# Optimization experiments

Measured on AMD Instinct MI355X. Metric: run time of the kernel, lower is better.

Reference implementation:

```python
import jax, jax.numpy as jnp
import numpy as np


def setup_inputs() -> dict:
    key = jax.random.key(0)
    ks = jax.random.split(key, 6)
    B, C, W, H = 8, 512, 64, 64
    return {
        "x": jax.random.normal(ks[0], (B, C, W, H), dtype=jnp.float32),
        "proj_query": jax.random.normal(ks[1], (C, W, H), dtype=jnp.float32),
        "key_w": jax.random.normal(ks[2], (C, C), dtype=jnp.float32) * 0.02,
        "key_b": jax.random.normal(ks[3], (C,), dtype=jnp.float32) * 0.02,
        "value_w": jax.random.normal(ks[4], (C, C), dtype=jnp.float32) * 0.02,
        "value_b": jax.random.normal(ks[5], (C,), dtype=jnp.float32) * 0.02,
        "gamma": jnp.ones((1,), dtype=jnp.float32),
    }


def reference(x, proj_query, key_w, key_b, value_w, value_b, gamma):
    B, C, W, H = x.shape
    N = W * H
    # fixed memory query: (C, N); torch builds B x N x C via permute
    q = proj_query.reshape(C, N)
    # 1x1 convs == per-pixel channel matmuls
    k = jnp.einsum('oc,bchw->bohw', key_w, x) + key_b[None, :, None, None]
    v = jnp.einsum('oc,bchw->bohw', value_w, x) + value_b[None, :, None, None]
    k = k.reshape(B, C, N)
    v = v.reshape(B, C, N)
    # energy = bmm(key [B,C,N], query^T [N,C]) -> B x C x C (channel attention)
    energy = jnp.einsum('bcn,dn->bcd', k, q)
    attention = jax.nn.softmax(energy, axis=-1)
    # out = bmm(attention^T [B,C,C], value [B,C,N]) -> B x C x N
    out = jnp.einsum('bdc,bdn->bcn', attention, v)
    out = out.reshape(B, C, W, H)
    return gamma * out + x
```

## Files before the change

kernel.cpp:

```cpp
#include <hip/hip_runtime.h>

typedef unsigned short u16;
typedef unsigned int u32;
typedef _Float16 f16x8 __attribute__((ext_vector_type(8)));
typedef float f32x4 __attribute__((ext_vector_type(4)));

#define LDST 40

__device__ __forceinline__ u16 f2h(float f) {
  union { _Float16 h; u16 u; } c; c.h = (_Float16)f; return c.u;
}
__device__ __forceinline__ float h2f(u16 v) {
  union { u16 u; _Float16 h; } c; c.u = v; return (float)c.h;
}

__device__ __forceinline__ f32x4 mfma16(f16x8 a, f16x8 b, f32x4 c) {
  return __builtin_amdgcn_mfma_f32_16x16x32_f16(a, b, c, 0, 0, 0);
}

__device__ __forceinline__ void ld8f(const float* s, u16* o) {
  float4 a = *(const float4*)s;
  float4 b = *(const float4*)(s + 4);
  o[0] = f2h(a.x); o[1] = f2h(a.y); o[2] = f2h(a.z); o[3] = f2h(a.w);
  o[4] = f2h(b.x); o[5] = f2h(b.y); o[6] = f2h(b.z); o[7] = f2h(b.w);
}

template<int TM, int TN, bool NNB>
__device__ __forceinline__ void gemm_core(const u16* A, int lda, const u16* B, int ldb,
                                          int ksteps, u16* sA, u16* sB, f32x4 acc[TM][TN]) {
  const int t = threadIdx.x;
  const int lane = t & 63, wave = t >> 6;
  const int wm = wave >> 1, wn = wave & 1;
  const int m16 = lane & 15, q4 = lane >> 4;
  constexpr int BM = TM * 32, BN = TN * 32;

  for (int kt = 0; kt < ksteps; ++kt) {
    __syncthreads();
#pragma unroll
    for (int p = 0; p < BM / 64; ++p) {
      int flat = (p * 256 + t) * 8;
      int row = flat >> 5, col = flat & 31;
      *(int4*)&sA[row * LDST + col] = *(const int4*)&A[(size_t)row * lda + col];
    }
    if constexpr (!NNB) {
#pragma unroll
      for (int p = 0; p < BN / 64; ++p) {
        int flat = (p * 256 + t) * 8;
        int row = flat >> 5, col = flat & 31;
        *(int4*)&sB[row * LDST + col] = *(const int4*)&B[(size_t)row * ldb + col];
      }
    } else {
      int kk = (t >> 4) * 2, nn = (t & 15) * 8;
      const u16* src = B + (size_t)kk * ldb + nn;
      u16 a0[8], a1[8];
      *(int4*)a0 = *(const int4*)src;
      *(int4*)a1 = *(const int4*)(src + ldb);
#pragma unroll
      for (int e = 0; e < 8; ++e) {
        int n = nn + e;
        int kf = kk ^ (((n >> 3) & 3) << 3);
        *(u32*)&sB[n * LDST + kf] = (u32)a0[e] | ((u32)a1[e] << 16);
      }
    }
    __syncthreads();

    f16x8 af[TM], bv[TN];
#pragma unroll
    for (int i = 0; i < TM; ++i)
      af[i] = *(const f16x8*)&sA[(wm * TM * 16 + i * 16 + m16) * LDST + q4 * 8];
#pragma unroll
    for (int j = 0; j < TN; ++j) {
      int n = wn * TN * 16 + j * 16 + m16;
      int kf = NNB ? ((q4 * 8) ^ (((n >> 3) & 3) << 3)) : (q4 * 8);
      bv[j] = *(const f16x8*)&sB[n * LDST + kf];
    }
#pragma unroll
    for (int i = 0; i < TM; ++i)
#pragma unroll
      for (int j = 0; j < TN; ++j)
        acc[i][j] = mfma16(af[i], bv[j], acc[i][j]);

    A += 32;
    B += NNB ? (size_t)32 * ldb : (size_t)32;
  }
}

__global__ __launch_bounds__(256) void cvt_x_kernel(const float* __restrict__ x, u16* __restrict__ xh) {
  size_t i = ((size_t)blockIdx.x * 256 + threadIdx.x) * 8;
  u16 o[8];
  ld8f(x + i, o);
  *(int4*)&xh[i] = *(int4*)o;
}

__global__ __launch_bounds__(256) void cvt_q_kernel(const float* __restrict__ q, u16* __restrict__ qh,
                                                    float* __restrict__ qs) {
  int row = blockIdx.x, t = threadIdx.x;
  float s = 0.f;
#pragma unroll
  for (int p = 0; p < 2; ++p) {
    size_t i = (size_t)row * 4096 + p * 2048 + t * 8;
    u16 o[8];
    ld8f(q + i, o);
#pragma unroll
    for (int e = 0; e < 8; ++e) s += h2f(o[e]);
    *(int4*)&qh[i] = *(int4*)o;
  }
  for (int off = 32; off; off >>= 1) s += __shfl_xor(s, off);
  __shared__ float wsum[4];
  if ((t & 63) == 0) wsum[t >> 6] = s;
  __syncthreads();
  if (t == 0) qs[row] = wsum[0] + wsum[1] + wsum[2] + wsum[3];
}

__global__ __launch_bounds__(256) void prep_kernel(const float* __restrict__ vw, u16* __restrict__ vwT,
                                                   const float* __restrict__ kw, u16* __restrict__ kwh,
                                                   float* __restrict__ beta) {
  int blk = blockIdx.x, t = threadIdx.x;
  if (blk < 256) {
    __shared__ u16 sT[32 * 33];
    int bx = blk & 15, by = blk >> 4;
#pragma unroll
    for (int p = 0; p < 4; ++p) {
      int idx = p * 256 + t; int r = idx >> 5, c = idx & 31;
      sT[r * 33 + c] = f2h(vw[(size_t)(by * 32 + r) * 512 + bx * 32 + c]);
    }
    __syncthreads();
#pragma unroll
    for (int p = 0; p < 4; ++p) {
      int idx = p * 256 + t; int r = idx >> 5, c = idx & 31;
      vwT[(size_t)(bx * 32 + r) * 512 + by * 32 + c] = sT[c * 33 + r];
    }
  } else if (blk < 384) {
    size_t i = ((size_t)(blk - 256) * 256 + t) * 8;
    u16 o[8];
    ld8f(kw + i, o);
    *(int4*)&kwh[i] = *(int4*)o;
  } else {
    for (int i = t; i < 4096; i += 256) beta[i] = 0.f;
  }
}

__global__ __launch_bounds__(256) void sgemm_kernel(const u16* __restrict__ qh, const u16* __restrict__ xh,
                                                    u16* __restrict__ Sh) {
  __shared__ u16 sA[64 * LDST], sB[64 * LDST];
  int rt = blockIdx.x, jt = blockIdx.y;
  f32x4 acc[2][2];
#pragma unroll
  for (int i = 0; i < 2; ++i)
#pragma unroll
    for (int j = 0; j < 2; ++j) acc[i][j] = (f32x4){0.f, 0.f, 0.f, 0.f};
  gemm_core<2, 2, false>(qh + (size_t)jt * 64 * 4096, 4096,
                         xh + (size_t)rt * 64 * 4096, 4096, 128, sA, sB, acc);

  const int t = threadIdx.x, lane = t & 63, wave = t >> 6;
  const int wm = wave >> 1, wn = wave & 1, m16 = lane & 15, q4 = lane >> 4;
  int b = (rt * 64) >> 9, o0 = (rt * 64) & 511;
  u16* Ob = Sh + (size_t)b * 262144;
#pragma unroll
  for (int i = 0; i < 2; ++i)
#pragma unroll
    for (int j = 0; j < 2; ++j)
#pragma unroll
      for (int r = 0; r < 4; ++r) {
        int y = jt * 64 + wm * 32 + i * 16 + q4 * 4 + r;
        int o = o0 + wn * 32 + j * 16 + m16;
        Ob[(size_t)y * 512 + o] = f2h(acc[i][j][r]);
      }
}

__global__ __launch_bounds__(256) void egemm_kernel(const u16* __restrict__ kwh, const u16* __restrict__ Sh,
                                                    float* __restrict__ E) {
  __shared__ u16 sA[64 * LDST], sB[64 * LDST];
  int xt = blockIdx.x >> 3, yt = blockIdx.x & 7, b = blockIdx.y;
  f32x4 acc[2][2];
#pragma unroll
  for (int i = 0; i < 2; ++i)
#pragma unroll
    for (int j = 0; j < 2; ++j) acc[i][j] = (f32x4){0.f, 0.f, 0.f, 0.f};
  gemm_core<2, 2, false>(kwh + (size_t)xt * 64 * 512, 512,
                         Sh + (size_t)b * 262144 + (size_t)yt * 64 * 512, 512, 16, sA, sB, acc);

  const int t = threadIdx.x, lane = t & 63, wave = t >> 6;
  const int wm = wave >> 1, wn = wave & 1, m16 = lane & 15, q4 = lane >> 4;
  float* O = E + ((size_t)b * 512 + xt * 64) * 512 + yt * 64;
#pragma unroll
  for (int i = 0; i < 2; ++i)
#pragma unroll
    for (int j = 0; j < 2; ++j)
#pragma unroll
      for (int r = 0; r < 4; ++r) {
        int row = wm * 32 + i * 16 + q4 * 4 + r;
        int col = wn * 32 + j * 16 + m16;
        O[(size_t)row * 512 + col] = acc[i][j][r];
      }
}

__global__ __launch_bounds__(256) void softmax_kernel(const float* __restrict__ E, const float* __restrict__ qs,
                                                      const float* __restrict__ kb, const float* __restrict__ vb,
                                                      u16* __restrict__ attT, float* __restrict__ beta) {
  __shared__ float sE[16 * 516];
  __shared__ float sM[16], sS[16];
  int i0 = blockIdx.x * 16, b = blockIdx.y, t = threadIdx.x;
  const float* Eb = E + ((size_t)b * 512 + i0) * 512;
  for (int ch = 0; ch < 32; ++ch) {
    int idx = ch * 256 + t;
    int row = idx >> 9, col = idx & 511;
    sE[row * 516 + col] = Eb[(size_t)row * 512 + col] + kb[i0 + row] * qs[col];
  }
  __syncthreads();
  {
    int row = t >> 4, sub = t & 15;
    float mx = -1e30f;
    for (int ii = 0; ii < 32; ++ii) mx = fmaxf(mx, sE[row * 516 + sub + ii * 16]);
    for (int off = 8; off; off >>= 1) mx = fmaxf(mx, __shfl_xor(mx, off));
    float sm = 0.f;
    for (int ii = 0; ii < 32; ++ii) sm += __expf(sE[row * 516 + sub + ii * 16] - mx);
    for (int off = 8; off; off >>= 1) sm += __shfl_xor(sm, off);
    if (sub == 0) { sM[row] = mx; sS[row] = 1.f / sm; }
  }
  __syncthreads();
  float vbr = vb[i0 + (t & 15)];
  u16* Ob = attT + (size_t)b * 262144;
  for (int ch = 0; ch < 32; ++ch) {
    int idx = ch * 256 + t;
    int r = idx & 15, j = idx >> 4;
    float a = __expf(sE[r * 516 + j] - sM[r]) * sS[r];
    Ob[(size_t)j * 512 + i0 + r] = f2h(a);
    float part = a * vbr;
    for (int off = 8; off; off >>= 1) part += __shfl_xor(part, off);
    if (r == 0) atomicAdd(&beta[b * 512 + j], part);
  }
}

__global__ __launch_bounds__(256) void wgemm_kernel(const u16* __restrict__ attT, const u16* __restrict__ vwT,
                                                    u16* __restrict__ W) {
  __shared__ u16 sA[64 * LDST], sB[64 * LDST];
  int ct = blockIdx.x >> 3, ot = blockIdx.x & 7, b = blockIdx.y;
  f32x4 acc[2][2];
#pragma unroll
  for (int i = 0; i < 2; ++i)
#pragma unroll
    for (int j = 0; j < 2; ++j) acc[i][j] = (f32x4){0.f, 0.f, 0.f, 0.f};
  gemm_core<2, 2, false>(attT + (size_t)b * 262144 + (size_t)ct * 64 * 512, 512,
                         vwT + (size_t)ot * 64 * 512, 512, 16, sA, sB, acc);

  const int t = threadIdx.x, lane = t & 63, wave = t >> 6;
  const int wm = wave >> 1, wn = wave & 1, m16 = lane & 15, q4 = lane >> 4;
  u16* O = W + (size_t)b * 262144 + (size_t)(ct * 64) * 512 + ot * 64;
#pragma unroll
  for (int i = 0; i < 2; ++i)
#pragma unroll
    for (int j = 0; j < 2; ++j)
#pragma unroll
      for (int r = 0; r < 4; ++r) {
        int row = wm * 32 + i * 16 + q4 * 4 + r;
        int col = wn * 32 + j * 16 + m16;
        O[(size_t)row * 512 + col] = f2h(acc[i][j][r]);
      }
}

__global__ __launch_bounds__(256) void outgemm_kernel(const u16* __restrict__ W, const u16* __restrict__ xh,
                                                      const float* __restrict__ x, const float* __restrict__ beta,
                                                      const float* __restrict__ gm, float* __restrict__ out) {
  __shared__ u16 sA[128 * LDST], sB[128 * LDST];
  int nt = blockIdx.x, ct = blockIdx.y, b = blockIdx.z;
  f32x4 acc[4][4];
#pragma unroll
  for (int i = 0; i < 4; ++i)
#pragma unroll
    for (int j = 0; j < 4; ++j) acc[i][j] = (f32x4){0.f, 0.f, 0.f, 0.f};
  gemm_core<4, 4, true>(W + (size_t)b * 262144 + (size_t)ct * 128 * 512, 512,
                        xh + (size_t)b * 2097152 + nt * 128, 4096, 16, sA, sB, acc);

  const int t = threadIdx.x, lane = t & 63, wave = t >> 6;
  const int wm = wave >> 1, wn = wave & 1, m16 = lane & 15, q4 = lane >> 4;
  float g = gm[0];
#pragma unroll
  for (int i = 0; i < 4; ++i)
#pragma unroll
    for (int j = 0; j < 4; ++j)
#pragma unroll
      for (int r = 0; r < 4; ++r) {
        int c = ct * 128 + wm * 64 + i * 16 + q4 * 4 + r;
        int n = nt * 128 + wn * 64 + j * 16 + m16;
        size_t idx = (size_t)b * 2097152 + (size_t)c * 4096 + n;
        out[idx] = g * (acc[i][j][r] + beta[b * 512 + c]) + x[idx];
      }
}

extern "C" void kernel_launch(void* const* d_in, const int* in_sizes, int n_in,
                              void* d_out, int out_size, void* d_ws, size_t ws_size,
                              hipStream_t stream) {
  const float* x  = (const float*)d_in[0];
  const float* pq = (const float*)d_in[1];
  const float* kw = (const float*)d_in[2];
  const float* kb = (const float*)d_in[3];
  const float* vw = (const float*)d_in[4];
  const float* vb = (const float*)d_in[5];
  const float* gm = (const float*)d_in[6];
  float* out = (float*)d_out;

  char* ws = (char*)d_ws;
  u16*   xh   = (u16*)(ws);
  u16*   qh   = (u16*)(ws + (32ull << 20));
  u16*   Sh   = (u16*)(ws + (36ull << 20));
  u16*   W    = (u16*)(ws + (36ull << 20));
  float* E    = (float*)(ws + (40ull << 20));
  u16*   attT = (u16*)(ws + (48ull << 20));
  u16*   kwh  = (u16*)(ws + (52ull << 20));
  u16*   vwT  = (u16*)(ws + (52ull << 20) + 524288);
  char*  sm   = ws + (53ull << 20);
  float* qs   = (float*)(sm);
  float* beta = (float*)(sm + 4096);

  cvt_x_kernel<<<dim3(8192), 256, 0, stream>>>(x, xh);
  cvt_q_kernel<<<dim3(512), 256, 0, stream>>>(pq, qh, qs);
  prep_kernel<<<dim3(385), 256, 0, stream>>>(vw, vwT, kw, kwh, beta);
  sgemm_kernel<<<dim3(64, 8), 256, 0, stream>>>(qh, xh, Sh);
  egemm_kernel<<<dim3(64, 8), 256, 0, stream>>>(kwh, Sh, E);
  softmax_kernel<<<dim3(32, 8), 256, 0, stream>>>(E, qs, kb, vb, attT, beta);
  wgemm_kernel<<<dim3(64, 8), 256, 0, stream>>>(attT, vwT, W);
  outgemm_kernel<<<dim3(32, 4, 8), 256, 0, stream>>>(W, xh, x, beta, gm, out);
}
```

Measured before the change: 262.7 us.

## Fuse conversions into prep kernel, read fp32 directly in S-GEMM, pre-transpose x

Merges the separate x and query conversion kernels into one prep kernel that writes x transposed to channel-last fp16 and only computes the query row sums. The S-GEMM now loads fp32 x and query directly and converts them while staging into LDS, so it no longer needs the fp16 copies of x or the query. The output GEMM reads the pre-transposed x with plain row loads, dropping its swizzled in-LDS transpose path. In exchange the S-GEMM reads twice as many bytes per tile and repeats the fp32-to-fp16 conversion for every tile reuse, and the prep kernel adds an LDS-based transpose.

Result: slower. 288.7 us (+9.9%).

```diff
diff --git a/kernel.cpp b/kernel.cpp
--- a/kernel.cpp
+++ b/kernel.cpp
@@ -25,14 +25,15 @@
   o[4] = f2h(b.x); o[5] = f2h(b.y); o[6] = f2h(b.z); o[7] = f2h(b.w);
 }
 
-template<int TM, int TN, bool NNB>
-__device__ __forceinline__ void gemm_core(const u16* A, int lda, const u16* B, int ldb,
+template<int TM, int TN, bool AF32, bool BF32>
+__device__ __forceinline__ void gemm_core(const void* Ab, int lda, const void* Bb, int ldb,
                                           int ksteps, u16* sA, u16* sB, f32x4 acc[TM][TN]) {
   const int t = threadIdx.x;
   const int lane = t & 63, wave = t >> 6;
   const int wm = wave >> 1, wn = wave & 1;
   const int m16 = lane & 15, q4 = lane >> 4;
   constexpr int BM = TM * 32, BN = TN * 32;
+  size_t ko = 0;
 
   for (int kt = 0; kt < ksteps; ++kt) {
     __syncthreads();
@@ -40,27 +41,19 @@
     for (int p = 0; p < BM / 64; ++p) {
       int flat = (p * 256 + t) * 8;
       int row = flat >> 5, col = flat & 31;
-      *(int4*)&sA[row * LDST + col] = *(const int4*)&A[(size_t)row * lda + col];
-    }
-    if constexpr (!NNB) {
-#pragma unroll
-      for (int p = 0; p < BN / 64; ++p) {
-        int flat = (p * 256 + t) * 8;
-        int row = flat >> 5, col = flat & 31;
-        *(int4*)&sB[row * LDST + col] = *(const int4*)&B[(size_t)row * ldb + col];
-      }
-    } else {
-      int kk = (t >> 4) * 2, nn = (t & 15) * 8;
-      const u16* src = B + (size_t)kk * ldb + nn;
-      u16 a0[8], a1[8];
-      *(int4*)a0 = *(const int4*)src;
-      *(int4*)a1 = *(const int4*)(src + ldb);
-#pragma unroll
-      for (int e = 0; e < 8; ++e) {
-        int n = nn + e;
-        int kf = kk ^ (((n >> 3) & 3) << 3);
-        *(u32*)&sB[n * LDST + kf] = (u32)a0[e] | ((u32)a1[e] << 16);
-      }
+      u16 o[8];
+      if constexpr (AF32) ld8f((const float*)Ab + (size_t)row * lda + ko + col, o);
+      else *(int4*)o = *(const int4*)((const u16*)Ab + (size_t)row * lda + ko + col);
+      *(int4*)&sA[row * LDST + col] = *(int4*)o;
+    }
+#pragma unroll
+    for (int p = 0; p < BN / 64; ++p) {
+      int flat = (p * 256 + t) * 8;
+      int row = flat >> 5, col = flat & 31;
+      u16 o[8];
+      if constexpr (BF32) ld8f((const float*)Bb + (size_t)row * ldb + ko + col, o);
+      else *(int4*)o = *(const int4*)((const u16*)Bb + (size_t)row * ldb + ko + col);
+      *(int4*)&sB[row * LDST + col] = *(int4*)o;
     }
     __syncthreads();
 
@@ -69,69 +62,76 @@
     for (int i = 0; i < TM; ++i)
       af[i] = *(const f16x8*)&sA[(wm * TM * 16 + i * 16 + m16) * LDST + q4 * 8];
 #pragma unroll
-    for (int j = 0; j < TN; ++j) {
-      int n = wn * TN * 16 + j * 16 + m16;
-      int kf = NNB ? ((q4 * 8) ^ (((n >> 3) & 3) << 3)) : (q4 * 8);
-      bv[j] = *(const f16x8*)&sB[n * LDST + kf];
-    }
+    for (int j = 0; j < TN; ++j)
+      bv[j] = *(const f16x8*)&sB[(wn * TN * 16 + j * 16 + m16) * LDST + q4 * 8];
 #pragma unroll
     for (int i = 0; i < TM; ++i)
 #pragma unroll
       for (int j = 0; j < TN; ++j)
         acc[i][j] = mfma16(af[i], bv[j], acc[i][j]);
 
-    A += 32;
-    B += NNB ? (size_t)32 * ldb : (size_t)32;
-  }
-}
-
-__global__ __launch_bounds__(256) void cvt_x_kernel(const float* __restrict__ x, u16* __restrict__ xh) {
-  size_t i = ((size_t)blockIdx.x * 256 + threadIdx.x) * 8;
-  u16 o[8];
-  ld8f(x + i, o);
-  *(int4*)&xh[i] = *(int4*)o;
-}
-
-__global__ __launch_bounds__(256) void cvt_q_kernel(const float* __restrict__ q, u16* __restrict__ qh,
-                                                    float* __restrict__ qs) {
-  int row = blockIdx.x, t = threadIdx.x;
-  float s = 0.f;
-#pragma unroll
-  for (int p = 0; p < 2; ++p) {
-    size_t i = (size_t)row * 4096 + p * 2048 + t * 8;
-    u16 o[8];
-    ld8f(q + i, o);
-#pragma unroll
-    for (int e = 0; e < 8; ++e) s += h2f(o[e]);
-    *(int4*)&qh[i] = *(int4*)o;
-  }
-  for (int off = 32; off; off >>= 1) s += __shfl_xor(s, off);
-  __shared__ float wsum[4];
-  if ((t & 63) == 0) wsum[t >> 6] = s;
-  __syncthreads();
-  if (t == 0) qs[row] = wsum[0] + wsum[1] + wsum[2] + wsum[3];
-}
-
-__global__ __launch_bounds__(256) void prep_kernel(const float* __restrict__ vw, u16* __restrict__ vwT,
+    ko += 32;
+  }
+}
+
+__global__ __launch_bounds__(256) void prep_kernel(const float* __restrict__ x, u16* __restrict__ xhT,
+                                                   const float* __restrict__ q, float* __restrict__ qs,
+                                                   const float* __restrict__ vw, u16* __restrict__ vwT,
                                                    const float* __restrict__ kw, u16* __restrict__ kwh,
                                                    float* __restrict__ beta) {
   int blk = blockIdx.x, t = threadIdx.x;
-  if (blk < 256) {
-    __shared__ u16 sT[32 * 33];
-    int bx = blk & 15, by = blk >> 4;
+  if (blk < 4096) {
+    __shared__ u16 sT[64 * 72];
+    int b = blk >> 9, rem = blk & 511, nt = rem & 63, ot = rem >> 6;
+    const float* xb = x + (size_t)b * 2097152 + (size_t)(ot * 64) * 4096 + nt * 64;
+#pragma unroll
+    for (int p = 0; p < 4; ++p) {
+      int idx = p * 256 + t;
+      int r = idx >> 4, c4 = (idx & 15) * 4;
+      float4 v = *(const float4*)&xb[(size_t)r * 4096 + c4];
+      u16 o4[4] = {f2h(v.x), f2h(v.y), f2h(v.z), f2h(v.w)};
+      *(uint2*)&sT[r * 72 + c4] = *(uint2*)o4;
+    }
+    __syncthreads();
+#pragma unroll
+    for (int p = 0; p < 2; ++p) {
+      int idx = p * 256 + t;
+      int r2 = idx >> 3, c8 = (idx & 7) * 8;
+      u16 o[8];
+#pragma unroll
+      for (int e = 0; e < 8; ++e) o[e] = sT[(c8 + e) * 72 + r2];
+      *(int4*)&xhT[(size_t)b * 2097152 + (size_t)(nt * 64 + r2) * 512 + ot * 64 + c8] = *(int4*)o;
+    }
+  } else if (blk < 4608) {
+    int row = blk - 4096;
+    float s = 0.f;
+#pragma unroll
+    for (int p = 0; p < 4; ++p) {
+      float4 v = *(const float4*)&q[(size_t)row * 4096 + p * 1024 + t * 4];
+      s += v.x + v.y + v.z + v.w;
+    }
+    for (int off = 32; off; off >>= 1) s += __shfl_xor(s, off);
+    __shared__ float wsum[4];
+    if ((t & 63) == 0) wsum[t >> 6] = s;
+    __syncthreads();
+    if (t == 0) qs[row] = wsum[0] + wsum[1] + wsum[2] + wsum[3];
+  } else if (blk < 4864) {
+    __shared__ u16 sV[32 * 33];
+    int rel = blk - 4608;
+    int bx = rel & 15, by = rel >> 4;
 #pragma unroll
     for (int p = 0; p < 4; ++p) {
       int idx = p * 256 + t; int r = idx >> 5, c = idx & 31;
-      sT[r * 33 + c] = f2h(vw[(size_t)(by * 32 + r) * 512 + bx * 32 + c]);
+      sV[r * 33 + c] = f2h(vw[(size_t)(by * 32 + r) * 512 + bx * 32 + c]);
     }
     __syncthreads();
 #pragma unroll
     for (int p = 0; p < 4; ++p) {
       int idx = p * 256 + t; int r = idx >> 5, c = idx & 31;
-      vwT[(size_t)(bx * 32 + r) * 512 + by * 32 + c] = sT[c * 33 + r];
-    }
-  } else if (blk < 384) {
-    size_t i = ((size_t)(blk - 256) * 256 + t) * 8;
+      vwT[(size_t)(bx * 32 + r) * 512 + by * 32 + c] = sV[c * 33 + r];
+    }
+  } else if (blk < 4992) {
+    size_t i = ((size_t)(blk - 4864) * 256 + t) * 8;
     u16 o[8];
     ld8f(kw + i, o);
     *(int4*)&kwh[i] = *(int4*)o;
@@ -140,7 +140,7 @@
   }
 }
 
-__global__ __launch_bounds__(256) void sgemm_kernel(const u16* __restrict__ qh, const u16* __restrict__ xh,
+__global__ __launch_bounds__(256) void sgemm_kernel(const float* __restrict__ q, const float* __restrict__ x,
                                                     u16* __restrict__ Sh) {
   __shared__ u16 sA[64 * LDST], sB[64 * LDST];
   int rt = blockIdx.x, jt = blockIdx.y;
@@ -149,8 +149,8 @@
   for (int i = 0; i < 2; ++i)
 #pragma unroll
     for (int j = 0; j < 2; ++j) acc[i][j] = (f32x4){0.f, 0.f, 0.f, 0.f};
-  gemm_core<2, 2, false>(qh + (size_t)jt * 64 * 4096, 4096,
-                         xh + (size_t)rt * 64 * 4096, 4096, 128, sA, sB, acc);
+  gemm_core<2, 2, true, true>(q + (size_t)jt * 64 * 4096, 4096,
+                              x + (size_t)rt * 64 * 4096, 4096, 128, sA, sB, acc);
 
   const int t = threadIdx.x, lane = t & 63, wave = t >> 6;
   const int wm = wave >> 1, wn = wave & 1, m16 = lane & 15, q4 = lane >> 4;
@@ -177,8 +177,8 @@
   for (int i = 0; i < 2; ++i)
 #pragma unroll
     for (int j = 0; j < 2; ++j) acc[i][j] = (f32x4){0.f, 0.f, 0.f, 0.f};
-  gemm_core<2, 2, false>(kwh + (size_t)xt * 64 * 512, 512,
-                         Sh + (size_t)b * 262144 + (size_t)yt * 64 * 512, 512, 16, sA, sB, acc);
+  gemm_core<2, 2, false, false>(kwh + (size_t)xt * 64 * 512, 512,
+                                Sh + (size_t)b * 262144 + (size_t)yt * 64 * 512, 512, 16, sA, sB, acc);
 
   const int t = threadIdx.x, lane = t & 63, wave = t >> 6;
   const int wm = wave >> 1, wn = wave & 1, m16 = lane & 15, q4 = lane >> 4;
@@ -241,8 +241,8 @@
   for (int i = 0; i < 2; ++i)
 #pragma unroll
     for (int j = 0; j < 2; ++j) acc[i][j] = (f32x4){0.f, 0.f, 0.f, 0.f};
-  gemm_core<2, 2, false>(attT + (size_t)b * 262144 + (size_t)ct * 64 * 512, 512,
-                         vwT + (size_t)ot * 64 * 512, 512, 16, sA, sB, acc);
+  gemm_core<2, 2, false, false>(attT + (size_t)b * 262144 + (size_t)ct * 64 * 512, 512,
+                                vwT + (size_t)ot * 64 * 512, 512, 16, sA, sB, acc);
 
   const int t = threadIdx.x, lane = t & 63, wave = t >> 6;
   const int wm = wave >> 1, wn = wave & 1, m16 = lane & 15, q4 = lane >> 4;
@@ -259,7 +259,7 @@
       }
 }
 
-__global__ __launch_bounds__(256) void outgemm_kernel(const u16* __restrict__ W, const u16* __restrict__ xh,
+__global__ __launch_bounds__(256) void outgemm_kernel(const u16* __restrict__ W, const u16* __restrict__ xhT,
                                                       const float* __restrict__ x, const float* __restrict__ beta,
                                                       const float* __restrict__ gm, float* __restrict__ out) {
   __shared__ u16 sA[128 * LDST], sB[128 * LDST];
@@ -269,8 +269,8 @@
   for (int i = 0; i < 4; ++i)
 #pragma unroll
     for (int j = 0; j < 4; ++j) acc[i][j] = (f32x4){0.f, 0.f, 0.f, 0.f};
-  gemm_core<4, 4, true>(W + (size_t)b * 262144 + (size_t)ct * 128 * 512, 512,
-                        xh + (size_t)b * 2097152 + nt * 128, 4096, 16, sA, sB, acc);
+  gemm_core<4, 4, false, false>(W + (size_t)b * 262144 + (size_t)ct * 128 * 512, 512,
+                                xhT + (size_t)b * 2097152 + (size_t)nt * 128 * 512, 512, 16, sA, sB, acc);
 
   const int t = threadIdx.x, lane = t & 63, wave = t >> 6;
   const int wm = wave >> 1, wn = wave & 1, m16 = lane & 15, q4 = lane >> 4;
@@ -301,24 +301,21 @@
   float* out = (float*)d_out;
 
   char* ws = (char*)d_ws;
-  u16*   xh   = (u16*)(ws);
-  u16*   qh   = (u16*)(ws + (32ull << 20));
-  u16*   Sh   = (u16*)(ws + (36ull << 20));
-  u16*   W    = (u16*)(ws + (36ull << 20));
-  float* E    = (float*)(ws + (40ull << 20));
-  u16*   attT = (u16*)(ws + (48ull << 20));
-  u16*   kwh  = (u16*)(ws + (52ull << 20));
-  u16*   vwT  = (u16*)(ws + (52ull << 20) + 524288);
-  char*  sm   = ws + (53ull << 20);
+  u16*   xhT  = (u16*)(ws);
+  u16*   Sh   = (u16*)(ws + (32ull << 20));
+  u16*   W    = (u16*)(ws + (32ull << 20));
+  float* E    = (float*)(ws + (36ull << 20));
+  u16*   attT = (u16*)(ws + (44ull << 20));
+  u16*   kwh  = (u16*)(ws + (48ull << 20));
+  u16*   vwT  = (u16*)(ws + (48ull << 20) + 524288);
+  char*  sm   = ws + (49ull << 20);
   float* qs   = (float*)(sm);
   float* beta = (float*)(sm + 4096);
 
-  cvt_x_kernel<<<dim3(8192), 256, 0, stream>>>(x, xh);
-  cvt_q_kernel<<<dim3(512), 256, 0, stream>>>(pq, qh, qs);
-  prep_kernel<<<dim3(385), 256, 0, stream>>>(vw, vwT, kw, kwh, beta);
-  sgemm_kernel<<<dim3(64, 8), 256, 0, stream>>>(qh, xh, Sh);
+  prep_kernel<<<dim3(4993), 256, 0, stream>>>(x, xhT, pq, qs, vw, vwT, kw, kwh, beta);
+  sgemm_kernel<<<dim3(64, 8), 256, 0, stream>>>(pq, x, Sh);
   egemm_kernel<<<dim3(64, 8), 256, 0, stream>>>(kwh, Sh, E);
   softmax_kernel<<<dim3(32, 8), 256, 0, stream>>>(E, qs, kb, vb, attT, beta);
   wgemm_kernel<<<dim3(64, 8), 256, 0, stream>>>(attT, vwT, W);
-  outgemm_kernel<<<dim3(32, 4, 8), 256, 0, stream>>>(W, xh, x, beta, gm, out);
-}
+  outgemm_kernel<<<dim3(32, 4, 8), 256, 0, stream>>>(W, xhT, x, beta, gm, out);
+}
```
